# Kernel optimization log

Measured on AMD Instinct MI355X. Metric: run time of the kernel, lower is better.

Reference implementation:

```python
import jax, jax.numpy as jnp
import numpy as np

N, E, F_IN, H, C = 50000, 800000, 128, 128, 64


def setup_inputs() -> dict:
    key = jax.random.key(0)
    ks = jax.random.split(key, 10)
    s = lambda f: np.float32(1.0 / np.sqrt(f))
    return {
        "x": jax.random.normal(ks[0], (N, F_IN), jnp.float32),
        "edge_index": jax.random.randint(ks[1], (2, E), 0, N, dtype=jnp.int64),
        # SAGEConv1: lin_l (on aggregated neighbors, with bias) + lin_r (on root, no bias)
        "W1l": jax.random.normal(ks[2], (F_IN, H), jnp.float32) * s(F_IN),
        "b1l": jnp.zeros((H,), jnp.float32),
        "W1r": jax.random.normal(ks[3], (F_IN, H), jnp.float32) * s(F_IN),
        # SAGEConv2
        "W2l": jax.random.normal(ks[4], (H, C), jnp.float32) * s(H),
        "b2l": jnp.zeros((C,), jnp.float32),
        "W2r": jax.random.normal(ks[5], (H, C), jnp.float32) * s(H),
        # GCNConv
        "Wg": jax.random.normal(ks[6], (C, C), jnp.float32) * s(C),
        "bg": jnp.zeros((C,), jnp.float32),
    }


def sage_conv(x, edge_index, Wl, bl, Wr):
    # PyG SAGEConv (mean aggr): out = lin_l(mean_{j in N(i)} x_j) + lin_r(x_i)
    n = x.shape[0]
    src, dst = edge_index[0], edge_index[1]
    agg = jax.ops.segment_sum(x[src], dst, num_segments=n)  # [N, F]
    cnt = jax.ops.segment_sum(jnp.ones((src.shape[0],), x.dtype), dst, num_segments=n)
    mean = agg / jnp.maximum(cnt, 1.0)[:, None]
    return mean @ Wl + bl + x @ Wr


def gcn_conv(x, edge_index, W, b):
    # PyG GCNConv: add self loops, symmetric normalization D^-1/2 A D^-1/2
    n = x.shape[0]
    loop = jnp.arange(n, dtype=edge_index.dtype)
    src = jnp.concatenate([edge_index[0], loop])
    dst = jnp.concatenate([edge_index[1], loop])
    deg = jax.ops.segment_sum(jnp.ones((src.shape[0],), x.dtype), dst, num_segments=n)
    dinv = jnp.where(deg > 0, jax.lax.rsqrt(jnp.maximum(deg, 1e-12)), 0.0)
    norm = dinv[src] * dinv[dst]  # [E+N]
    xw = x @ W
    out = jax.ops.segment_sum(xw[src] * norm[:, None], dst, num_segments=n)
    return out + b


def reference(x, edge_index, W1l, b1l, W1r, W2l, b2l, W2r, Wg, bg):
    h = jax.nn.relu(sage_conv(x, edge_index, W1l, b1l, W1r))
    # dropout is identity in eval mode
    h = sage_conv(h, edge_index, W2l, b2l, W2r)
    h = jax.nn.softmax(h, axis=1)  # activate='softmax'
    return gcn_conv(h, edge_index, Wg, bg)
```

## Files before the change

kernel.cpp:

```cpp
#include <hip/hip_runtime.h>
#include <hip/hip_fp16.h>
#include <math.h>


typedef __attribute__((ext_vector_type(8))) short bf16x8;
typedef __attribute__((ext_vector_type(4))) float f32x4;
typedef __attribute__((ext_vector_type(2))) float f32v2;

__device__ inline unsigned short f32_bf16_hi(float f) {
    unsigned int u = __builtin_bit_cast(unsigned int, f);
    u = (u + 0x7FFFu + ((u >> 16) & 1u)) >> 16;
    return (unsigned short)u;
}
__device__ inline float bf16_to_f32(unsigned short h) {
    unsigned int u = ((unsigned int)h) << 16;
    return __builtin_bit_cast(float, u);
}

union H8 { float4 f4; __half2 h[4]; };

__device__ inline void dec16(uint4 u, float* a0, float* a1) {
    f32v2 x0 = __builtin_amdgcn_cvt_pk_f32_fp8(u.x, false);
    f32v2 x1 = __builtin_amdgcn_cvt_pk_f32_fp8(u.x, true);
    f32v2 y0 = __builtin_amdgcn_cvt_pk_f32_fp8(u.y, false);
    f32v2 y1 = __builtin_amdgcn_cvt_pk_f32_fp8(u.y, true);
    a0[0] += x0[0]; a0[1] += x0[1]; a0[2] += x1[0]; a0[3] += x1[1];
    a0[4] += y0[0]; a0[5] += y0[1]; a0[6] += y1[0]; a0[7] += y1[1];
    f32v2 z0 = __builtin_amdgcn_cvt_pk_f32_fp8(u.z, false);
    f32v2 z1 = __builtin_amdgcn_cvt_pk_f32_fp8(u.z, true);
    f32v2 w0 = __builtin_amdgcn_cvt_pk_f32_fp8(u.w, false);
    f32v2 w1 = __builtin_amdgcn_cvt_pk_f32_fp8(u.w, true);
    a1[0] += z0[0]; a1[1] += z0[1]; a1[2] += z1[0]; a1[3] += z1[1];
    a1[4] += w0[0]; a1[5] += w0[1]; a1[6] += w1[0]; a1[7] += w1[1];
}

__device__ inline unsigned char enc8(float v) {
    int w = __builtin_amdgcn_cvt_pk_fp8_f32(v, v, 0, false);
    return (unsigned char)(w & 0xff);
}

__global__ void count_kernel(const int* __restrict__ dst, int* __restrict__ off,
                             int E, int NB, int BK) {
    __shared__ int hist[256];
    int t = threadIdx.x;
    hist[t] = 0;
    __syncthreads();
    int base = blockIdx.x * 8192;
    for (int i = t; i < 8192; i += 256) {
        int e = base + i;
        if (e < E) atomicAdd(&hist[dst[e] >> 8], 1);
    }
    __syncthreads();
    if (t < BK) off[1 + t * NB + blockIdx.x] = hist[t];
    if (blockIdx.x == 0 && t == 0) off[0] = 0;
}

__global__ void scan_reduce_kernel(const int* __restrict__ data, int* __restrict__ bsum, int n) {
    __shared__ int red[256];
    int t = threadIdx.x;
    int base = blockIdx.x * 2048 + t * 8;
    int s = 0;
    if (base + 8 <= n) {
        int4 a = *(const int4*)(data + base);
        int4 b = *(const int4*)(data + base + 4);
        s = a.x + a.y + a.z + a.w + b.x + b.y + b.z + b.w;
    } else {
        for (int i = 0; i < 8; ++i)
            if (base + i < n) s += data[base + i];
    }
    red[t] = s;
    __syncthreads();
    for (int off = 128; off > 0; off >>= 1) {
        if (t < off) red[t] += red[t + off];
        __syncthreads();
    }
    if (t == 0) bsum[blockIdx.x] = red[0];
}

__global__ void scan_offsets_kernel(int* __restrict__ bsum, int B) {
    if (threadIdx.x == 0 && blockIdx.x == 0) {
        int run = 0;
        for (int i = 0; i < B; ++i) { int v = bsum[i]; bsum[i] = run; run += v; }
    }
}

__global__ void scan_final_kernel(int* __restrict__ data, const int* __restrict__ bsum, int n) {
    __shared__ int tsum[256];
    int t = threadIdx.x;
    int base = blockIdx.x * 2048 + t * 8;
    int v[8];
    int s = 0;
#pragma unroll
    for (int i = 0; i < 8; ++i) {
        v[i] = (base + i < n) ? data[base + i] : 0;
        s += v[i];
    }
    tsum[t] = s;
    for (int off = 1; off < 256; off <<= 1) {
        __syncthreads();
        int u = (t >= off) ? tsum[t - off] : 0;
        __syncthreads();
        tsum[t] += u;
    }
    __syncthreads();
    int run = bsum[blockIdx.x] + tsum[t] - s;
#pragma unroll
    for (int i = 0; i < 8; ++i) {
        run += v[i];
        if (base + i < n) data[base + i] = run;
    }
}

__global__ void partition_kernel(const int* __restrict__ src, const int* __restrict__ dst,
                                 const int* __restrict__ off, unsigned* __restrict__ ebuf,
                                 int E, int NB, int BK) {
    __shared__ int cur[256];
    int t = threadIdx.x;
    if (t < BK) cur[t] = off[t * NB + blockIdx.x];
    __syncthreads();
    int base = blockIdx.x * 8192;
    for (int i = t; i < 8192; i += 256) {
        int e = base + i;
        if (e < E) {
            int d = dst[e];
            int pos = atomicAdd(&cur[d >> 8], 1);
            ebuf[pos] = ((unsigned)src[e] << 8) | (unsigned)(d & 255);
        }
    }
}

__global__ void finalize_kernel(const unsigned* __restrict__ ebuf, const int* __restrict__ off,
                                int* __restrict__ col, int* __restrict__ rowptr,
                                float* __restrict__ dinv, int N, int NB, int E) {
    __shared__ int hist[256], scn[256], cur[256];
    int b = blockIdx.x, t = threadIdx.x;
    int base = off[b * NB];
    int end  = off[(b + 1) * NB];
    int M = end - base;
    hist[t] = 0;
    __syncthreads();
    for (int i = t; i < M; i += 256) atomicAdd(&hist[ebuf[base + i] & 255u], 1);
    __syncthreads();
    scn[t] = hist[t];
    for (int o = 1; o < 256; o <<= 1) {
        __syncthreads();
        int u = (t >= o) ? scn[t - o] : 0;
        __syncthreads();
        scn[t] += u;
    }
    __syncthreads();
    int excl = scn[t] - hist[t];
    int node = b * 256 + t;
    if (node < N) {
        rowptr[node] = base + excl;
        dinv[node] = rsqrtf((float)(hist[t] + 1));
    }
    if (b == 0 && t == 0) rowptr[N] = E;
    cur[t] = base + excl;
    __syncthreads();
    for (int i = t; i < M; i += 256) {
        unsigned w = ebuf[base + i];
        int pos = atomicAdd(&cur[w & 255u], 1);
        col[pos] = (int)(w >> 8);
    }
}

__global__ void packw_kernel(const float* __restrict__ W1l, const float* __restrict__ W1r,
                             const float* __restrict__ W2l, const float* __restrict__ W2r,
                             const float* __restrict__ Wg,
                             unsigned short* __restrict__ p1h, unsigned short* __restrict__ p1l,
                             unsigned short* __restrict__ p2h, unsigned short* __restrict__ p2l,
                             unsigned short* __restrict__ p3h, unsigned short* __restrict__ p3l) {
    int which = blockIdx.y;
    const float* W;
    unsigned short *hi, *lo;
    int K, Mp, colOff, T;
    if (which == 0)      { W = W1l; hi = p1h; lo = p1l; K = 128; Mp = 128; colOff = 0;   T = 16; }
    else if (which == 1) { W = W1r; hi = p1h; lo = p1l; K = 128; Mp = 128; colOff = 128; T = 16; }
    else if (which == 2) { W = W2l; hi = p2h; lo = p2l; K = 128; Mp = 64;  colOff = 0;   T = 8;  }
    else if (which == 3) { W = W2r; hi = p2h; lo = p2l; K = 128; Mp = 64;  colOff = 64;  T = 8;  }
    else                 { W = Wg;  hi = p3h; lo = p3l; K = 64;  Mp = 64;  colOff = 0;   T = 4;  }
    int idx = blockIdx.x * blockDim.x + threadIdx.x;
    if (idx >= K * Mp) return;
    int k = idx / Mp, m = idx % Mp;
    float w = W[(size_t)k * Mp + m];
    int colI = colOff + m;
    int s = k >> 5, kk = k & 31, qq = kk >> 3, j = kk & 7;
    int tt = colI >> 4, n = colI & 15;
    int lane = qq * 16 + n;
    size_t pos = ((size_t)(s * T + tt) * 64 + lane) * 8 + j;
    unsigned short h = f32_bf16_hi(w);
    hi[pos] = h;
    lo[pos] = f32_bf16_hi(w - bf16_to_f32(h));
}

__launch_bounds__(256)
__global__ void gemm1_kernel(const float* __restrict__ A,
                             const unsigned short* __restrict__ Whi,
                             const unsigned short* __restrict__ Wlo,
                             unsigned char* __restrict__ outA8, __half* __restrict__ outB, int N) {
    constexpr int Ttot = 16, TB = 8;
    __shared__ __align__(16) unsigned char pk[4][16][128];
    const int lane = threadIdx.x & 63;
    const int wave = threadIdx.x >> 6;
    const int m = lane & 15, q = lane >> 4;
    const int t0 = blockIdx.y * TB;
    const int row0 = blockIdx.x * 64 + wave * 16;
    int arow = row0 + m;
    if (arow >= N) arow = N - 1;
    const float* ap = A + (size_t)arow * 128 + q * 8;

    float av[4][8];
#pragma unroll
    for (int s = 0; s < 4; ++s) {
        *(float4*)(av[s])     = *(const float4*)(ap + s * 32);
        *(float4*)(av[s] + 4) = *(const float4*)(ap + s * 32 + 4);
    }
    bf16x8 ahi[4], alo[4];
#pragma unroll
    for (int s = 0; s < 4; ++s)
#pragma unroll
        for (int i = 0; i < 8; ++i) {
            unsigned short h = f32_bf16_hi(av[s][i]);
            ahi[s][i] = (short)h;
            alo[s][i] = (short)f32_bf16_hi(av[s][i] - bf16_to_f32(h));
        }

    f32x4 acc[TB];
#pragma unroll
    for (int t = 0; t < TB; ++t) acc[t] = (f32x4)(0.f);
    const bf16x8* whp = (const bf16x8*)Whi;
    const bf16x8* wlp = (const bf16x8*)Wlo;
#pragma unroll
    for (int s = 0; s < 4; ++s) {
        const int base = (s * Ttot + t0) * 64 + lane;
#pragma unroll
        for (int t = 0; t < TB; ++t) {
            bf16x8 wh = whp[base + t * 64];
            bf16x8 wl = wlp[base + t * 64];
            acc[t] = __builtin_amdgcn_mfma_f32_16x16x32_bf16(ahi[s], wh, acc[t], 0, 0, 0);
            acc[t] = __builtin_amdgcn_mfma_f32_16x16x32_bf16(alo[s], wh, acc[t], 0, 0, 0);
            acc[t] = __builtin_amdgcn_mfma_f32_16x16x32_bf16(ahi[s], wl, acc[t], 0, 0, 0);
        }
    }

    if (blockIdx.y == 0) {
#pragma unroll
        for (int r = 0; r < 4; ++r) {
            int row = q * 4 + r;
            int sw = (row & 3) << 5;
#pragma unroll
            for (int t = 0; t < 8; t += 2) {
                int w = __builtin_amdgcn_cvt_pk_fp8_f32(acc[t][r], acc[t + 1][r], 0, false);
                int off = (t >> 1) * 8 + (m & 7);
                int c0 = ((2 * t + (m >> 3)) & 3) * 32 + off;
                int c1 = ((2 * t + 2 + (m >> 3)) & 3) * 32 + off;
                pk[wave][row][c0 ^ sw] = (unsigned char)(w & 0xff);
                pk[wave][row][c1 ^ sw] = (unsigned char)((w >> 8) & 0xff);
            }
        }
        __syncthreads();
        int rr = lane >> 2, qt = lane & 3;
        int grow = row0 + rr;
        if (grow < N) {
            const unsigned char* srcp = &pk[wave][rr][(qt ^ (rr & 3)) * 32];
            uint4 v0 = *(const uint4*)(srcp);
            uint4 v1 = *(const uint4*)(srcp + 16);
            *(uint4*)(outA8 + (size_t)grow * 128 + qt * 32) = v0;
            *(uint4*)(outA8 + (size_t)grow * 128 + qt * 32 + 16) = v1;
        }
    } else {
#pragma unroll
        for (int r = 0; r < 4; ++r) {
            int row = row0 + q * 4 + r;
            if (row < N) {
#pragma unroll
                for (int t = 0; t < TB; ++t) {
                    int c = (t0 + t) * 16 + m - 128;
                    outB[(size_t)row * 128 + c] = __float2half(acc[t][r]);
                }
            }
        }
    }
}

__launch_bounds__(256)
__global__ void sage2_fused_kernel(const unsigned char* __restrict__ p8, const __half* __restrict__ q16,
                                   const int* __restrict__ rowptr, const int* __restrict__ col,
                                   const float* __restrict__ b1l,
                                   const unsigned short* __restrict__ Whi,
                                   const unsigned short* __restrict__ Wlo,
                                   unsigned char* __restrict__ r8, __half* __restrict__ s16, int N) {
    __shared__ float part[4][64][16];
    const int lane = threadIdx.x & 63;
    const int wave = threadIdx.x >> 6;
    const int pairH = wave & 1;
    const int grp   = wave >> 1;
    const int m = lane & 15, q = lane >> 4;
    const int row0 = blockIdx.x * 32 + grp * 16;
    int node = row0 + m;
    int nclamp = (node < N) ? node : (N - 1);
    int sAll = rowptr[nclamp];
    int eAll = (node < N) ? rowptr[nclamp + 1] : sAll;
    int deg  = eAll - sAll;
    int half0 = (deg + 1) >> 1;
    int sIdx = sAll + (pairH ? half0 : 0);
    int eIdx = pairH ? eAll : (sAll + half0);

    float acc[4][8];
#pragma unroll
    for (int s = 0; s < 4; ++s)
#pragma unroll
        for (int i = 0; i < 8; ++i) acc[s][i] = 0.f;

    const unsigned char* pb = p8 + q * 32;
    int ptr = sIdx;
    for (; ptr + 4 <= eIdx; ptr += 4) {
        int j0 = col[ptr], j1 = col[ptr + 1], j2 = col[ptr + 2], j3 = col[ptr + 3];
        uint4 uA[4], uB[4];
        uA[0] = *(const uint4*)(pb + (size_t)j0 * 128);
        uB[0] = *(const uint4*)(pb + (size_t)j0 * 128 + 16);
        uA[1] = *(const uint4*)(pb + (size_t)j1 * 128);
        uB[1] = *(const uint4*)(pb + (size_t)j1 * 128 + 16);
        uA[2] = *(const uint4*)(pb + (size_t)j2 * 128);
        uB[2] = *(const uint4*)(pb + (size_t)j2 * 128 + 16);
        uA[3] = *(const uint4*)(pb + (size_t)j3 * 128);
        uB[3] = *(const uint4*)(pb + (size_t)j3 * 128 + 16);
#pragma unroll
        for (int e = 0; e < 4; ++e) {
            dec16(uA[e], acc[0], acc[1]);
            dec16(uB[e], acc[2], acc[3]);
        }
    }
    for (; ptr < eIdx; ++ptr) {
        int j0 = col[ptr];
        uint4 uA = *(const uint4*)(pb + (size_t)j0 * 128);
        uint4 uB = *(const uint4*)(pb + (size_t)j0 * 128 + 16);
        dec16(uA, acc[0], acc[1]);
        dec16(uB, acc[2], acc[3]);
    }

    float* ap = &acc[0][0];
    const int swz = lane & 3;
#pragma unroll
    for (int c = 0; c < 2; ++c) {
        if (c) __syncthreads();
#pragma unroll
        for (int sl = 0; sl < 4; ++sl)
            *(float4*)&part[wave][lane][(sl ^ swz) * 4] =
                *(const float4*)(ap + (c * 4 + sl) * 4);
        __syncthreads();
#pragma unroll
        for (int sl = 0; sl < 4; ++sl) {
            float4 pv = *(const float4*)&part[wave ^ 1][lane][(sl ^ swz) * 4];
            int g = (c * 4 + sl) * 4;
            ap[g]     += pv.x;
            ap[g + 1] += pv.y;
            ap[g + 2] += pv.z;
            ap[g + 3] += pv.w;
        }
    }

    float inv = 1.0f / fmaxf((float)deg, 1.0f);
    bf16x8 ahi[4], alo[4];
#pragma unroll
    for (int s = 0; s < 4; ++s) {
        H8 qv;
        qv.f4 = *(const float4*)(q16 + (size_t)nclamp * 128 + s * 32 + q * 8);
        float bv[8];
        *(float4*)(bv)     = *(const float4*)(b1l + s * 32 + q * 8);
        *(float4*)(bv + 4) = *(const float4*)(b1l + s * 32 + q * 8 + 4);
#pragma unroll
        for (int i = 0; i < 8; ++i) {
            float qf = __half2float(((const __half*)&qv)[i]);
            float h = fmaxf(acc[s][i] * inv + qf + bv[i], 0.f);
            unsigned short hb = f32_bf16_hi(h);
            ahi[s][i] = (short)hb;
            alo[s][i] = (short)f32_bf16_hi(h - bf16_to_f32(hb));
        }
    }

    f32x4 accm[4];
#pragma unroll
    for (int t = 0; t < 4; ++t) accm[t] = (f32x4)(0.f);
    const bf16x8* whp = (const bf16x8*)Whi;
    const bf16x8* wlp = (const bf16x8*)Wlo;
#pragma unroll
    for (int s = 0; s < 4; ++s) {
        const int base = (s * 8 + pairH * 4) * 64 + lane;
#pragma unroll
        for (int t = 0; t < 4; ++t) {
            bf16x8 wh = whp[base + t * 64];
            bf16x8 wl = wlp[base + t * 64];
            accm[t] = __builtin_amdgcn_mfma_f32_16x16x32_bf16(ahi[s], wh, accm[t], 0, 0, 0);
            accm[t] = __builtin_amdgcn_mfma_f32_16x16x32_bf16(alo[s], wh, accm[t], 0, 0, 0);
            accm[t] = __builtin_amdgcn_mfma_f32_16x16x32_bf16(ahi[s], wl, accm[t], 0, 0, 0);
        }
    }
#pragma unroll
    for (int r = 0; r < 4; ++r) {
        int row = row0 + q * 4 + r;
        if (row < N) {
            if (pairH == 0) {
#pragma unroll
                for (int t = 0; t < 4; ++t) {
                    int c = t * 16 + m;
                    int pos = ((c >> 3) & 3) * 16 + ((c >> 5) & 1) * 8 + (c & 7);
                    r8[(size_t)row * 64 + pos] = enc8(accm[t][r]);
                }
            } else {
#pragma unroll
                for (int t = 0; t < 4; ++t) {
                    int c = t * 16 + m;
                    s16[(size_t)row * 64 + c] = __float2half(accm[t][r]);
                }
            }
        }
    }
}

__launch_bounds__(256)
__global__ void gcn_prep_fused_kernel(const unsigned char* __restrict__ r8, const __half* __restrict__ s16,
                                      const int* __restrict__ rowptr, const int* __restrict__ col,
                                      const float* __restrict__ b2l,
                                      const unsigned short* __restrict__ Whi,
                                      const unsigned short* __restrict__ Wlo,
                                      const float* __restrict__ dinv,
                                      __half* __restrict__ tpA, __half* __restrict__ tpB, int N) {
    __shared__ float part[4][64][16];
    const int lane = threadIdx.x & 63;
    const int wave = threadIdx.x >> 6;
    const int pairH = wave & 1;
    const int grp   = wave >> 1;
    const int m = lane & 15, q = lane >> 4;
    const int row0 = blockIdx.x * 32 + grp * 16;
    int node = row0 + m;
    int nclamp = (node < N) ? node : (N - 1);
    int sAll = rowptr[nclamp];
    int eAll = (node < N) ? rowptr[nclamp + 1] : sAll;
    int deg  = eAll - sAll;
    int half0 = (deg + 1) >> 1;
    int sIdx = sAll + (pairH ? half0 : 0);
    int eIdx = pairH ? eAll : (sAll + half0);

    float acc[2][8];
#pragma unroll
    for (int s = 0; s < 2; ++s)
#pragma unroll
        for (int i = 0; i < 8; ++i) acc[s][i] = 0.f;

    const unsigned char* rb = r8 + q * 16;
    int ptr = sIdx;
    for (; ptr + 4 <= eIdx; ptr += 4) {
        int j0 = col[ptr], j1 = col[ptr + 1], j2 = col[ptr + 2], j3 = col[ptr + 3];
        uint4 u0 = *(const uint4*)(rb + (size_t)j0 * 64);
        uint4 u1 = *(const uint4*)(rb + (size_t)j1 * 64);
        uint4 u2 = *(const uint4*)(rb + (size_t)j2 * 64);
        uint4 u3 = *(const uint4*)(rb + (size_t)j3 * 64);
        dec16(u0, acc[0], acc[1]);
        dec16(u1, acc[0], acc[1]);
        dec16(u2, acc[0], acc[1]);
        dec16(u3, acc[0], acc[1]);
    }
    for (; ptr < eIdx; ++ptr) {
        int j0 = col[ptr];
        uint4 u0 = *(const uint4*)(rb + (size_t)j0 * 64);
        dec16(u0, acc[0], acc[1]);
    }

    float* ap = &acc[0][0];
    const int swz = lane & 3;
#pragma unroll
    for (int sl = 0; sl < 4; ++sl)
        *(float4*)&part[wave][lane][(sl ^ swz) * 4] = *(const float4*)(ap + sl * 4);
    __syncthreads();
#pragma unroll
    for (int sl = 0; sl < 4; ++sl) {
        float4 pv = *(const float4*)&part[wave ^ 1][lane][(sl ^ swz) * 4];
        ap[sl * 4]     += pv.x;
        ap[sl * 4 + 1] += pv.y;
        ap[sl * 4 + 2] += pv.z;
        ap[sl * 4 + 3] += pv.w;
    }

    float inv = 1.0f / fmaxf((float)deg, 1.0f);
    float v[2][8];
    float mx = -1e30f;
#pragma unroll
    for (int s = 0; s < 2; ++s) {
        H8 sv;
        sv.f4 = *(const float4*)(s16 + (size_t)nclamp * 64 + s * 32 + q * 8);
        float bv[8];
        *(float4*)(bv)     = *(const float4*)(b2l + s * 32 + q * 8);
        *(float4*)(bv + 4) = *(const float4*)(b2l + s * 32 + q * 8 + 4);
#pragma unroll
        for (int i = 0; i < 8; ++i) {
            float sf = __half2float(((const __half*)&sv)[i]);
            v[s][i] = acc[s][i] * inv + sf + bv[i];
            mx = fmaxf(mx, v[s][i]);
        }
    }
    mx = fmaxf(mx, __shfl_xor(mx, 16, 64));
    mx = fmaxf(mx, __shfl_xor(mx, 32, 64));
    float sm = 0.f;
#pragma unroll
    for (int s = 0; s < 2; ++s)
#pragma unroll
        for (int i = 0; i < 8; ++i) {
            v[s][i] = expf(v[s][i] - mx);
            sm += v[s][i];
        }
    sm += __shfl_xor(sm, 16, 64);
    sm += __shfl_xor(sm, 32, 64);
    float is = 1.0f / sm;

    bf16x8 ahi[2], alo[2];
#pragma unroll
    for (int s = 0; s < 2; ++s)
#pragma unroll
        for (int i = 0; i < 8; ++i) {
            float h = v[s][i] * is;
            unsigned short hb = f32_bf16_hi(h);
            ahi[s][i] = (short)hb;
            alo[s][i] = (short)f32_bf16_hi(h - bf16_to_f32(hb));
        }

    f32x4 accm[2];
#pragma unroll
    for (int t = 0; t < 2; ++t) accm[t] = (f32x4)(0.f);
    const bf16x8* whp = (const bf16x8*)Whi;
    const bf16x8* wlp = (const bf16x8*)Wlo;
#pragma unroll
    for (int s = 0; s < 2; ++s) {
        const int base = (s * 4 + pairH * 2) * 64 + lane;
#pragma unroll
        for (int t = 0; t < 2; ++t) {
            bf16x8 wh = whp[base + t * 64];
            bf16x8 wl = wlp[base + t * 64];
            accm[t] = __builtin_amdgcn_mfma_f32_16x16x32_bf16(ahi[s], wh, accm[t], 0, 0, 0);
            accm[t] = __builtin_amdgcn_mfma_f32_16x16x32_bf16(alo[s], wh, accm[t], 0, 0, 0);
            accm[t] = __builtin_amdgcn_mfma_f32_16x16x32_bf16(ahi[s], wl, accm[t], 0, 0, 0);
        }
    }
    __half* plane = pairH ? tpB : tpA;
#pragma unroll
    for (int r = 0; r < 4; ++r) {
        int row = row0 + q * 4 + r;
        if (row < N) {
            float sc = dinv[row];
#pragma unroll
            for (int t = 0; t < 2; ++t) {
                int c = t * 16 + m;
                plane[(size_t)row * 32 + c] = __float2half(accm[t][r] * sc);
            }
        }
    }
}

__global__ void gcn_agg_kernel(const __half* __restrict__ tpP,
                               const int* __restrict__ rowptr, const int* __restrict__ col,
                               const float* __restrict__ dinv, const float* __restrict__ bg,
                               float* __restrict__ out, int N, int fOff) {
    int node = blockIdx.x * 4 + (threadIdx.x >> 6);
    if (node >= N) return;
    int lane = threadIdx.x & 63;
    int f2 = lane & 15;
    int ep = lane >> 4;
    int s = rowptr[node], e = rowptr[node + 1];
    float ax[4], ay[4];
#pragma unroll
    for (int k = 0; k < 4; ++k) { ax[k] = 0.f; ay[k] = 0.f; }
    int p = s;
    for (; p + 16 <= e; p += 16) {
#pragma unroll
        for (int k = 0; k < 4; ++k) {
            int j = col[p + 4 * k + ep];
            float2 f = __half22float2(*(const __half2*)(tpP + (size_t)j * 32 + 2 * f2));
            ax[k] += f.x;
            ay[k] += f.y;
        }
    }
    for (int t = p + ep; t < e; t += 4) {
        int j = col[t];
        float2 f = __half22float2(*(const __half2*)(tpP + (size_t)j * 32 + 2 * f2));
        ax[0] += f.x;
        ay[0] += f.y;
    }
    float sx = (ax[0] + ax[1]) + (ax[2] + ax[3]);
    float sy = (ay[0] + ay[1]) + (ay[2] + ay[3]);
    sx += __shfl_xor(sx, 16, 64); sx += __shfl_xor(sx, 32, 64);
    sy += __shfl_xor(sy, 16, 64); sy += __shfl_xor(sy, 32, 64);
    if (ep == 0) {
        float2 selfv = __half22float2(*(const __half2*)(tpP + (size_t)node * 32 + 2 * f2));
        float di = dinv[node];
        float2 o;
        o.x = (sx + selfv.x) * di + bg[fOff + 2 * f2];
        o.y = (sy + selfv.y) * di + bg[fOff + 2 * f2 + 1];
        *(float2*)(out + (size_t)node * 64 + fOff + 2 * f2) = o;
    }
}

extern "C" void kernel_launch(void* const* d_in, const int* in_sizes, int n_in,
                              void* d_out, int out_size, void* d_ws, size_t ws_size,
                              hipStream_t stream) {
    const float* x = (const float*)d_in[0];
    const int* ei = (const int*)d_in[1];
    const float* W1l = (const float*)d_in[2];
    const float* b1l = (const float*)d_in[3];
    const float* W1r = (const float*)d_in[4];
    const float* W2l = (const float*)d_in[5];
    const float* b2l = (const float*)d_in[6];
    const float* W2r = (const float*)d_in[7];
    const float* Wg  = (const float*)d_in[8];
    const float* bg  = (const float*)d_in[9];

    const int N = in_sizes[0] / 128;
    const int E = in_sizes[1] / 2;
    const int* srcp = ei;
    const int* dstp = ei + E;

    const int NB = (E + 8191) / 8192;
    const int BK = (N + 255) >> 8;
    const int len = BK * NB;

    float* ws = (float*)d_ws;
    float* dinv = ws;
    unsigned char* p8 = (unsigned char*)(dinv + N);
    __half* q16 = (__half*)(p8 + (size_t)N * 128);
    unsigned char* r8 = (unsigned char*)(q16 + (size_t)N * 128);
    __half* s16 = (__half*)(r8 + (size_t)N * 64);
    __half* tpA = s16 + (size_t)N * 64;
    __half* tpB = tpA + (size_t)N * 32;
    int* rowptr = (int*)(tpB + (size_t)N * 32);
    int* off    = rowptr + (N + 1);
    int* colbuf = off + len + 2;
    unsigned* ebuf = (unsigned*)(colbuf + E);
    int* bsum   = (int*)(ebuf + E);
    uintptr_t up = (uintptr_t)(bsum + 32);
    up = (up + 15) & ~(uintptr_t)15;
    unsigned short* p1h = (unsigned short*)up;
    unsigned short* p1l = p1h + 32768;
    unsigned short* p2h = p1l + 32768;
    unsigned short* p2l = p2h + 16384;
    unsigned short* p3h = p2l + 16384;
    unsigned short* p3l = p3h + 4096;

    float* out = (float*)d_out;

    count_kernel<<<NB, 256, 0, stream>>>(dstp, off, E, NB, BK);
    const int sn = len + 1;
    const int SBs = (sn + 2047) / 2048;
    scan_reduce_kernel<<<SBs, 256, 0, stream>>>(off, bsum, sn);
    scan_offsets_kernel<<<1, 64, 0, stream>>>(bsum, SBs);
    scan_final_kernel<<<SBs, 256, 0, stream>>>(off, bsum, sn);
    partition_kernel<<<NB, 256, 0, stream>>>(srcp, dstp, off, ebuf, E, NB, BK);
    finalize_kernel<<<BK, 256, 0, stream>>>(ebuf, off, colbuf, rowptr, dinv, N, NB, E);

    packw_kernel<<<dim3(64, 5), 256, 0, stream>>>(W1l, W1r, W2l, W2r, Wg,
                                                  p1h, p1l, p2h, p2l, p3h, p3l);

    const int gb  = (N + 63) / 64;
    const int gbf = (N + 31) / 32;
    const int ab  = (N + 3) / 4;

    gemm1_kernel<<<dim3(gb, 2), 256, 0, stream>>>(x, p1h, p1l, p8, q16, N);

    sage2_fused_kernel<<<gbf, 256, 0, stream>>>(p8, q16, rowptr, colbuf, b1l,
                                                p2h, p2l, r8, s16, N);

    gcn_prep_fused_kernel<<<gbf, 256, 0, stream>>>(r8, s16, rowptr, colbuf, b2l,
                                                   p3h, p3l, dinv, tpA, tpB, N);

    gcn_agg_kernel<<<ab, 256, 0, stream>>>(tpA, rowptr, colbuf, dinv, bg, out, N, 0);
    gcn_agg_kernel<<<ab, 256, 0, stream>>>(tpB, rowptr, colbuf, dinv, bg, out, N, 32);
}
```

Measured before the change: 271.4 us.

## Replace two-level CSR build with atomic count/scan/scatter, widen gathers, merge GCN agg

Replaces the bucketed partition-based CSR construction (count, three-kernel scan, partition, finalize) with a global atomic degree count, a single-block scan and an atomic scatter, and fuses degree zeroing with weight packing. This cuts kernel launches but makes the neighbour order within each row nondeterministic and puts heavy global-atomic contention on the degree and cursor arrays. The aggregation loops in both fused kernels are unrolled to 8 edges to keep more gathers in flight. The two half-width GCN aggregation passes are merged into one over a 64-wide fp16 buffer, which halves the index reads.

```diff
diff --git a/kernel.cpp b/kernel.cpp
--- a/kernel.cpp
+++ b/kernel.cpp
@@ -39,139 +39,21 @@
     return (unsigned char)(w & 0xff);
 }
 
-__global__ void count_kernel(const int* __restrict__ dst, int* __restrict__ off,
-                             int E, int NB, int BK) {
-    __shared__ int hist[256];
-    int t = threadIdx.x;
-    hist[t] = 0;
-    __syncthreads();
-    int base = blockIdx.x * 8192;
-    for (int i = t; i < 8192; i += 256) {
-        int e = base + i;
-        if (e < E) atomicAdd(&hist[dst[e] >> 8], 1);
-    }
-    __syncthreads();
-    if (t < BK) off[1 + t * NB + blockIdx.x] = hist[t];
-    if (blockIdx.x == 0 && t == 0) off[0] = 0;
-}
-
-__global__ void scan_reduce_kernel(const int* __restrict__ data, int* __restrict__ bsum, int n) {
-    __shared__ int red[256];
-    int t = threadIdx.x;
-    int base = blockIdx.x * 2048 + t * 8;
-    int s = 0;
-    if (base + 8 <= n) {
-        int4 a = *(const int4*)(data + base);
-        int4 b = *(const int4*)(data + base + 4);
-        s = a.x + a.y + a.z + a.w + b.x + b.y + b.z + b.w;
-    } else {
-        for (int i = 0; i < 8; ++i)
-            if (base + i < n) s += data[base + i];
-    }
-    red[t] = s;
-    __syncthreads();
-    for (int off = 128; off > 0; off >>= 1) {
-        if (t < off) red[t] += red[t + off];
-        __syncthreads();
-    }
-    if (t == 0) bsum[blockIdx.x] = red[0];
-}
-
-__global__ void scan_offsets_kernel(int* __restrict__ bsum, int B) {
-    if (threadIdx.x == 0 && blockIdx.x == 0) {
-        int run = 0;
-        for (int i = 0; i < B; ++i) { int v = bsum[i]; bsum[i] = run; run += v; }
-    }
-}
-
-__global__ void scan_final_kernel(int* __restrict__ data, const int* __restrict__ bsum, int n) {
-    __shared__ int tsum[256];
-    int t = threadIdx.x;
-    int base = blockIdx.x * 2048 + t * 8;
-    int v[8];
-    int s = 0;
-#pragma unroll
-    for (int i = 0; i < 8; ++i) {
-        v[i] = (base + i < n) ? data[base + i] : 0;
-        s += v[i];
-    }
-    tsum[t] = s;
-    for (int off = 1; off < 256; off <<= 1) {
-        __syncthreads();
-        int u = (t >= off) ? tsum[t - off] : 0;
-        __syncthreads();
-        tsum[t] += u;
-    }
-    __syncthreads();
-    int run = bsum[blockIdx.x] + tsum[t] - s;
-#pragma unroll
-    for (int i = 0; i < 8; ++i) {
-        run += v[i];
-        if (base + i < n) data[base + i] = run;
-    }
-}
-
-__global__ void partition_kernel(const int* __restrict__ src, const int* __restrict__ dst,
-                                 const int* __restrict__ off, unsigned* __restrict__ ebuf,
-                                 int E, int NB, int BK) {
-    __shared__ int cur[256];
-    int t = threadIdx.x;
-    if (t < BK) cur[t] = off[t * NB + blockIdx.x];
-    __syncthreads();
-    int base = blockIdx.x * 8192;
-    for (int i = t; i < 8192; i += 256) {
-        int e = base + i;
-        if (e < E) {
-            int d = dst[e];
-            int pos = atomicAdd(&cur[d >> 8], 1);
-            ebuf[pos] = ((unsigned)src[e] << 8) | (unsigned)(d & 255);
-        }
-    }
-}
-
-__global__ void finalize_kernel(const unsigned* __restrict__ ebuf, const int* __restrict__ off,
-                                int* __restrict__ col, int* __restrict__ rowptr,
-                                float* __restrict__ dinv, int N, int NB, int E) {
-    __shared__ int hist[256], scn[256], cur[256];
-    int b = blockIdx.x, t = threadIdx.x;
-    int base = off[b * NB];
-    int end  = off[(b + 1) * NB];
-    int M = end - base;
-    hist[t] = 0;
-    __syncthreads();
-    for (int i = t; i < M; i += 256) atomicAdd(&hist[ebuf[base + i] & 255u], 1);
-    __syncthreads();
-    scn[t] = hist[t];
-    for (int o = 1; o < 256; o <<= 1) {
-        __syncthreads();
-        int u = (t >= o) ? scn[t - o] : 0;
-        __syncthreads();
-        scn[t] += u;
-    }
-    __syncthreads();
-    int excl = scn[t] - hist[t];
-    int node = b * 256 + t;
-    if (node < N) {
-        rowptr[node] = base + excl;
-        dinv[node] = rsqrtf((float)(hist[t] + 1));
-    }
-    if (b == 0 && t == 0) rowptr[N] = E;
-    cur[t] = base + excl;
-    __syncthreads();
-    for (int i = t; i < M; i += 256) {
-        unsigned w = ebuf[base + i];
-        int pos = atomicAdd(&cur[w & 255u], 1);
-        col[pos] = (int)(w >> 8);
-    }
-}
-
-__global__ void packw_kernel(const float* __restrict__ W1l, const float* __restrict__ W1r,
-                             const float* __restrict__ W2l, const float* __restrict__ W2r,
-                             const float* __restrict__ Wg,
-                             unsigned short* __restrict__ p1h, unsigned short* __restrict__ p1l,
-                             unsigned short* __restrict__ p2h, unsigned short* __restrict__ p2l,
-                             unsigned short* __restrict__ p3h, unsigned short* __restrict__ p3l) {
-    int which = blockIdx.y;
+__global__ void zero_pack_kernel(int* __restrict__ deg, int degLen, int ZB,
+                                 const float* __restrict__ W1l, const float* __restrict__ W1r,
+                                 const float* __restrict__ W2l, const float* __restrict__ W2r,
+                                 const float* __restrict__ Wg,
+                                 unsigned short* __restrict__ p1h, unsigned short* __restrict__ p1l,
+                                 unsigned short* __restrict__ p2h, unsigned short* __restrict__ p2l,
+                                 unsigned short* __restrict__ p3h, unsigned short* __restrict__ p3l) {
+    if ((int)blockIdx.x < ZB) {
+        int idx = (blockIdx.x * 256 + threadIdx.x) * 4;
+        if (idx + 4 <= degLen) *(int4*)(deg + idx) = make_int4(0, 0, 0, 0);
+        else for (int k = 0; k < 4 && idx + k < degLen; ++k) deg[idx + k] = 0;
+        return;
+    }
+    int pb = blockIdx.x - ZB;
+    int which = pb >> 6;
     const float* W;
     unsigned short *hi, *lo;
     int K, Mp, colOff, T;
@@ -180,7 +62,7 @@
     else if (which == 2) { W = W2l; hi = p2h; lo = p2l; K = 128; Mp = 64;  colOff = 0;   T = 8;  }
     else if (which == 3) { W = W2r; hi = p2h; lo = p2l; K = 128; Mp = 64;  colOff = 64;  T = 8;  }
     else                 { W = Wg;  hi = p3h; lo = p3l; K = 64;  Mp = 64;  colOff = 0;   T = 4;  }
-    int idx = blockIdx.x * blockDim.x + threadIdx.x;
+    int idx = (pb & 63) * 256 + threadIdx.x;
     if (idx >= K * Mp) return;
     int k = idx / Mp, m = idx % Mp;
     float w = W[(size_t)k * Mp + m];
@@ -192,6 +74,77 @@
     unsigned short h = f32_bf16_hi(w);
     hi[pos] = h;
     lo[pos] = f32_bf16_hi(w - bf16_to_f32(h));
+}
+
+__global__ void count_kernel(const int* __restrict__ dst, int* __restrict__ deg, int E) {
+    int base = (blockIdx.x * 256 + threadIdx.x) * 4;
+    if (base + 4 <= E && (E & 3) == 0) {
+        int4 d4 = *(const int4*)(dst + base);
+        atomicAdd(&deg[d4.x], 1);
+        atomicAdd(&deg[d4.y], 1);
+        atomicAdd(&deg[d4.z], 1);
+        atomicAdd(&deg[d4.w], 1);
+    } else {
+        for (int k = 0; k < 4; ++k) {
+            int e = base + k;
+            if (e < E) atomicAdd(&deg[dst[e]], 1);
+        }
+    }
+}
+
+__launch_bounds__(1024)
+__global__ void scan_kernel(const int* __restrict__ deg, int* __restrict__ rowptr,
+                            int* __restrict__ cursor, float* __restrict__ dinv,
+                            int N, int E, int CH) {
+    __shared__ int sums[1024];
+    int t = threadIdx.x;
+    int c0 = t * CH;
+    int s = 0;
+    for (int i = 0; i < CH; i += 4) {
+        int4 v = *(const int4*)(deg + c0 + i);
+        s += v.x + v.y + v.z + v.w;
+    }
+    sums[t] = s;
+    __syncthreads();
+    for (int o = 1; o < 1024; o <<= 1) {
+        int u = (t >= o) ? sums[t - o] : 0;
+        __syncthreads();
+        sums[t] += u;
+        __syncthreads();
+    }
+    int run = sums[t] - s;
+    for (int i = 0; i < CH; ++i) {
+        int idx = c0 + i;
+        if (idx < N) {
+            rowptr[idx] = run;
+            cursor[idx] = run;
+            int d = deg[idx];
+            dinv[idx] = rsqrtf((float)(d + 1));
+            run += d;
+        }
+    }
+    if (t == 0) rowptr[N] = E;
+}
+
+__global__ void scatter_kernel(const int* __restrict__ src, const int* __restrict__ dst,
+                               int* __restrict__ cursor, int* __restrict__ col, int E) {
+    int base = (blockIdx.x * 256 + threadIdx.x) * 4;
+    if (base + 4 <= E && (E & 3) == 0) {
+        int4 d4 = *(const int4*)(dst + base);
+        int4 s4 = *(const int4*)(src + base);
+        int p0 = atomicAdd(&cursor[d4.x], 1); col[p0] = s4.x;
+        int p1 = atomicAdd(&cursor[d4.y], 1); col[p1] = s4.y;
+        int p2 = atomicAdd(&cursor[d4.z], 1); col[p2] = s4.z;
+        int p3 = atomicAdd(&cursor[d4.w], 1); col[p3] = s4.w;
+    } else {
+        for (int k = 0; k < 4; ++k) {
+            int e = base + k;
+            if (e < E) {
+                int pos = atomicAdd(&cursor[dst[e]], 1);
+                col[pos] = src[e];
+            }
+        }
+    }
 }
 
 __launch_bounds__(256)
@@ -315,17 +268,32 @@
 
     const unsigned char* pb = p8 + q * 32;
     int ptr = sIdx;
+    for (; ptr + 8 <= eIdx; ptr += 8) {
+        int j[8];
+#pragma unroll
+        for (int e = 0; e < 8; ++e) j[e] = col[ptr + e];
+        uint4 uA[8], uB[8];
+#pragma unroll
+        for (int e = 0; e < 8; ++e) {
+            uA[e] = *(const uint4*)(pb + (size_t)j[e] * 128);
+            uB[e] = *(const uint4*)(pb + (size_t)j[e] * 128 + 16);
+        }
+#pragma unroll
+        for (int e = 0; e < 8; ++e) {
+            dec16(uA[e], acc[0], acc[1]);
+            dec16(uB[e], acc[2], acc[3]);
+        }
+    }
     for (; ptr + 4 <= eIdx; ptr += 4) {
-        int j0 = col[ptr], j1 = col[ptr + 1], j2 = col[ptr + 2], j3 = col[ptr + 3];
+        int j[4];
+#pragma unroll
+        for (int e = 0; e < 4; ++e) j[e] = col[ptr + e];
         uint4 uA[4], uB[4];
-        uA[0] = *(const uint4*)(pb + (size_t)j0 * 128);
-        uB[0] = *(const uint4*)(pb + (size_t)j0 * 128 + 16);
-        uA[1] = *(const uint4*)(pb + (size_t)j1 * 128);
-        uB[1] = *(const uint4*)(pb + (size_t)j1 * 128 + 16);
-        uA[2] = *(const uint4*)(pb + (size_t)j2 * 128);
-        uB[2] = *(const uint4*)(pb + (size_t)j2 * 128 + 16);
-        uA[3] = *(const uint4*)(pb + (size_t)j3 * 128);
-        uB[3] = *(const uint4*)(pb + (size_t)j3 * 128 + 16);
+#pragma unroll
+        for (int e = 0; e < 4; ++e) {
+            uA[e] = *(const uint4*)(pb + (size_t)j[e] * 128);
+            uB[e] = *(const uint4*)(pb + (size_t)j[e] * 128 + 16);
+        }
 #pragma unroll
         for (int e = 0; e < 4; ++e) {
             dec16(uA[e], acc[0], acc[1]);
@@ -426,7 +394,7 @@
                                       const unsigned short* __restrict__ Whi,
                                       const unsigned short* __restrict__ Wlo,
                                       const float* __restrict__ dinv,
-                                      __half* __restrict__ tpA, __half* __restrict__ tpB, int N) {
+                                      __half* __restrict__ tp16, int N) {
     __shared__ float part[4][64][16];
     const int lane = threadIdx.x & 63;
     const int wave = threadIdx.x >> 6;
@@ -451,16 +419,25 @@
 
     const unsigned char* rb = r8 + q * 16;
     int ptr = sIdx;
+    for (; ptr + 8 <= eIdx; ptr += 8) {
+        int j[8];
+#pragma unroll
+        for (int e = 0; e < 8; ++e) j[e] = col[ptr + e];
+        uint4 u[8];
+#pragma unroll
+        for (int e = 0; e < 8; ++e) u[e] = *(const uint4*)(rb + (size_t)j[e] * 64);
+#pragma unroll
+        for (int e = 0; e < 8; ++e) dec16(u[e], acc[0], acc[1]);
+    }
     for (; ptr + 4 <= eIdx; ptr += 4) {
-        int j0 = col[ptr], j1 = col[ptr + 1], j2 = col[ptr + 2], j3 = col[ptr + 3];
-        uint4 u0 = *(const uint4*)(rb + (size_t)j0 * 64);
-        uint4 u1 = *(const uint4*)(rb + (size_t)j1 * 64);
-        uint4 u2 = *(const uint4*)(rb + (size_t)j2 * 64);
-        uint4 u3 = *(const uint4*)(rb + (size_t)j3 * 64);
-        dec16(u0, acc[0], acc[1]);
-        dec16(u1, acc[0], acc[1]);
-        dec16(u2, acc[0], acc[1]);
-        dec16(u3, acc[0], acc[1]);
+        int j[4];
+#pragma unroll
+        for (int e = 0; e < 4; ++e) j[e] = col[ptr + e];
+        uint4 u[4];
+#pragma unroll
+        for (int e = 0; e < 4; ++e) u[e] = *(const uint4*)(rb + (size_t)j[e] * 64);
+#pragma unroll
+        for (int e = 0; e < 4; ++e) dec16(u[e], acc[0], acc[1]);
     }
     for (; ptr < eIdx; ++ptr) {
         int j0 = col[ptr];
@@ -542,7 +519,6 @@
             accm[t] = __builtin_amdgcn_mfma_f32_16x16x32_bf16(ahi[s], wl, accm[t], 0, 0, 0);
         }
     }
-    __half* plane = pairH ? tpB : tpA;
 #pragma unroll
     for (int r = 0; r < 4; ++r) {
         int row = row0 + q * 4 + r;
@@ -550,53 +526,53 @@
             float sc = dinv[row];
 #pragma unroll
             for (int t = 0; t < 2; ++t) {
-                int c = t * 16 + m;
-                plane[(size_t)row * 32 + c] = __float2half(accm[t][r] * sc);
+                int c = (pairH * 2 + t) * 16 + m;
+                tp16[(size_t)row * 64 + c] = __float2half(accm[t][r] * sc);
             }
         }
     }
 }
 
-__global__ void gcn_agg_kernel(const __half* __restrict__ tpP,
+__global__ void gcn_agg_kernel(const __half* __restrict__ tp,
                                const int* __restrict__ rowptr, const int* __restrict__ col,
                                const float* __restrict__ dinv, const float* __restrict__ bg,
-                               float* __restrict__ out, int N, int fOff) {
+                               float* __restrict__ out, int N) {
     int node = blockIdx.x * 4 + (threadIdx.x >> 6);
     if (node >= N) return;
     int lane = threadIdx.x & 63;
-    int f2 = lane & 15;
-    int ep = lane >> 4;
+    int f2 = lane & 31;
+    int ep = lane >> 5;
     int s = rowptr[node], e = rowptr[node + 1];
-    float ax[4], ay[4];
-#pragma unroll
-    for (int k = 0; k < 4; ++k) { ax[k] = 0.f; ay[k] = 0.f; }
+    float ax[8], ay[8];
+#pragma unroll
+    for (int k = 0; k < 8; ++k) { ax[k] = 0.f; ay[k] = 0.f; }
     int p = s;
     for (; p + 16 <= e; p += 16) {
 #pragma unroll
-        for (int k = 0; k < 4; ++k) {
-            int j = col[p + 4 * k + ep];
-            float2 f = __half22float2(*(const __half2*)(tpP + (size_t)j * 32 + 2 * f2));
+        for (int k = 0; k < 8; ++k) {
+            int j = col[p + 2 * k + ep];
+            float2 f = __half22float2(*(const __half2*)(tp + (size_t)j * 64 + 2 * f2));
             ax[k] += f.x;
             ay[k] += f.y;
         }
     }
-    for (int t = p + ep; t < e; t += 4) {
+    for (int t = p + ep; t < e; t += 2) {
         int j = col[t];
-        float2 f = __half22float2(*(const __half2*)(tpP + (size_t)j * 32 + 2 * f2));
+        float2 f = __half22float2(*(const __half2*)(tp + (size_t)j * 64 + 2 * f2));
         ax[0] += f.x;
         ay[0] += f.y;
     }
-    float sx = (ax[0] + ax[1]) + (ax[2] + ax[3]);
-    float sy = (ay[0] + ay[1]) + (ay[2] + ay[3]);
-    sx += __shfl_xor(sx, 16, 64); sx += __shfl_xor(sx, 32, 64);
-    sy += __shfl_xor(sy, 16, 64); sy += __shfl_xor(sy, 32, 64);
+    float sx = ((ax[0] + ax[1]) + (ax[2] + ax[3])) + ((ax[4] + ax[5]) + (ax[6] + ax[7]));
+    float sy = ((ay[0] + ay[1]) + (ay[2] + ay[3])) + ((ay[4] + ay[5]) + (ay[6] + ay[7]));
+    sx += __shfl_xor(sx, 32, 64);
+    sy += __shfl_xor(sy, 32, 64);
     if (ep == 0) {
-        float2 selfv = __half22float2(*(const __half2*)(tpP + (size_t)node * 32 + 2 * f2));
+        float2 selfv = __half22float2(*(const __half2*)(tp + (size_t)node * 64 + 2 * f2));
         float di = dinv[node];
         float2 o;
-        o.x = (sx + selfv.x) * di + bg[fOff + 2 * f2];
-        o.y = (sy + selfv.y) * di + bg[fOff + 2 * f2 + 1];
-        *(float2*)(out + (size_t)node * 64 + fOff + 2 * f2) = o;
+        o.x = (sx + selfv.x) * di + bg[2 * f2];
+        o.y = (sy + selfv.y) * di + bg[2 * f2 + 1];
+        *(float2*)(out + (size_t)node * 64 + 2 * f2) = o;
     }
 }
 
@@ -619,9 +595,8 @@
     const int* srcp = ei;
     const int* dstp = ei + E;
 
-    const int NB = (E + 8191) / 8192;
-    const int BK = (N + 255) >> 8;
-    const int len = BK * NB;
+    const int CH = (((N + 1023) / 1024) + 3) & ~3;
+    const int degLen = 1024 * CH;
 
     float* ws = (float*)d_ws;
     float* dinv = ws;
@@ -629,16 +604,18 @@
     __half* q16 = (__half*)(p8 + (size_t)N * 128);
     unsigned char* r8 = (unsigned char*)(q16 + (size_t)N * 128);
     __half* s16 = (__half*)(r8 + (size_t)N * 64);
-    __half* tpA = s16 + (size_t)N * 64;
-    __half* tpB = tpA + (size_t)N * 32;
-    int* rowptr = (int*)(tpB + (size_t)N * 32);
-    int* off    = rowptr + (N + 1);
-    int* colbuf = off + len + 2;
-    unsigned* ebuf = (unsigned*)(colbuf + E);
-    int* bsum   = (int*)(ebuf + E);
-    uintptr_t up = (uintptr_t)(bsum + 32);
-    up = (up + 15) & ~(uintptr_t)15;
-    unsigned short* p1h = (unsigned short*)up;
+    __half* tp16 = s16 + (size_t)N * 64;
+    uintptr_t up0 = (uintptr_t)(tp16 + (size_t)N * 64);
+    up0 = (up0 + 15) & ~(uintptr_t)15;
+    int* rowptr = (int*)up0;
+    uintptr_t up1 = (uintptr_t)(rowptr + (N + 1));
+    up1 = (up1 + 15) & ~(uintptr_t)15;
+    int* deg    = (int*)up1;
+    int* cursor = deg + degLen;
+    int* colbuf = cursor + N;
+    uintptr_t up2 = (uintptr_t)(colbuf + E);
+    up2 = (up2 + 15) & ~(uintptr_t)15;
+    unsigned short* p1h = (unsigned short*)up2;
     unsigned short* p1l = p1h + 32768;
     unsigned short* p2h = p1l + 32768;
     unsigned short* p2l = p2h + 16384;
@@ -647,30 +624,26 @@
 
     float* out = (float*)d_out;
 
-    count_kernel<<<NB, 256, 0, stream>>>(dstp, off, E, NB, BK);
-    const int sn = len + 1;
-    const int SBs = (sn + 2047) / 2048;
-    scan_reduce_kernel<<<SBs, 256, 0, stream>>>(off, bsum, sn);
-    scan_offsets_kernel<<<1, 64, 0, stream>>>(bsum, SBs);
-    scan_final_kernel<<<SBs, 256, 0, stream>>>(off, bsum, sn);
-    partition_kernel<<<NB, 256, 0, stream>>>(srcp, dstp, off, ebuf, E, NB, BK);
-    finalize_kernel<<<BK, 256, 0, stream>>>(ebuf, off, colbuf, rowptr, dinv, N, NB, E);
-
-    packw_kernel<<<dim3(64, 5), 256, 0, stream>>>(W1l, W1r, W2l, W2r, Wg,
-                                                  p1h, p1l, p2h, p2l, p3h, p3l);
-
+    const int ZB = (degLen + 1023) / 1024;
+    const int CB = (E + 1023) / 1024;
     const int gb  = (N + 63) / 64;
     const int gbf = (N + 31) / 32;
     const int ab  = (N + 3) / 4;
 
+    zero_pack_kernel<<<ZB + 320, 256, 0, stream>>>(deg, degLen, ZB,
+                                                   W1l, W1r, W2l, W2r, Wg,
+                                                   p1h, p1l, p2h, p2l, p3h, p3l);
+    count_kernel<<<CB, 256, 0, stream>>>(dstp, deg, E);
+    scan_kernel<<<1, 1024, 0, stream>>>(deg, rowptr, cursor, dinv, N, E, CH);
+    scatter_kernel<<<CB, 256, 0, stream>>>(srcp, dstp, cursor, colbuf, E);
+
     gemm1_kernel<<<dim3(gb, 2), 256, 0, stream>>>(x, p1h, p1l, p8, q16, N);
 
     sage2_fused_kernel<<<gbf, 256, 0, stream>>>(p8, q16, rowptr, colbuf, b1l,
                                                 p2h, p2l, r8, s16, N);
 
     gcn_prep_fused_kernel<<<gbf, 256, 0, stream>>>(r8, s16, rowptr, colbuf, b2l,
-                                                   p3h, p3l, dinv, tpA, tpB, N);
-
-    gcn_agg_kernel<<<ab, 256, 0, stream>>>(tpA, rowptr, colbuf, dinv, bg, out, N, 0);
-    gcn_agg_kernel<<<ab, 256, 0, stream>>>(tpB, rowptr, colbuf, dinv, bg, out, N, 32);
-}
+                                                   p3h, p3l, dinv, tp16, N);
+
+    gcn_agg_kernel<<<ab, 256, 0, stream>>>(tp16, rowptr, colbuf, dinv, bg, out, N);
+}
```

New measurement: 424.2 us. 1.56x slower.
